# Performance work log

Hardware: AMD Instinct MI355X
Metric: run time of the kernel (lower is better)

## Reference

```python
import jax, jax.numpy as jnp
import numpy as np

H = 0.1           # bandwidth
R = 1024          # pdf_resolution
Q = 2048          # quantile_sample_resolution
EPS = 1e-6
LOG_NORM_SQRT2PI = float(np.log(np.sqrt(2.0 * np.pi)))


def _grid(s):
    # s: (E, Q) samples -> (E, R) linspace(min, max) with 0.0 replaced by 1e-7
    mn = s.min(axis=1)
    mx = s.max(axis=1)
    t = mn[:, None] + (mx - mn)[:, None] * (jnp.arange(R, dtype=s.dtype) / (R - 1))
    return jnp.where(t != 0.0, t, jnp.asarray(1e-7, s.dtype))


def _logpdf(x, locs):
    # x: (E, B) kernel centers; locs: (E, R) eval points
    # log p(t) = logsumexp_b(-0.5 ((t - x_b)/h)^2) - log(B) - log(h * sqrt(2*pi))
    B = x.shape[1]
    z = (locs[:, :, None] - x[:, None, :]) / H          # (E, R, B)
    lse = jax.nn.logsumexp(-0.5 * z * z, axis=-1)       # (E, R)
    return lse - (np.log(B) + np.log(H) + LOG_NORM_SQRT2PI)


def _kde(inputs, bank, noise, comp_idx, sel, slot_idx):
    x = inputs.T                                         # (E, B)
    # mixture sampling: pick component, add Gaussian noise (scale = bandwidth)
    samples = jnp.take_along_axis(x, comp_idx, axis=1) + H * noise   # (E, Q)

    # current pdf over sample range
    t0 = _grid(samples)
    current = jnp.exp(_logpdf(x, t0))                    # (E, R)

    # per-feature bijector branch (0..5; branch 6 'Exp' is unreachable in TF
    # since tf.random.uniform maxval=6 is exclusive)
    selc = sel[:, None]
    s = samples
    s_safe = jnp.where(jnp.abs(s) < EPS, jnp.asarray(EPS, s.dtype), s)
    conds_s = [selc == i for i in range(6)]
    y = jnp.select(conds_s, [
        2.0 * s,                 # Scale(2)
        s - 3.0,                 # Shift(-3)
        1.0 / s_safe,            # Reciprocal
        0.8 * s + 5.0,           # Chain([Shift(5), Scale(0.8)])
        jax.nn.sigmoid(s),       # Sigmoid
        jax.nn.softplus(s),      # Softplus
    ])
    t1 = _grid(y)                                        # (E, R)
    yc01 = jnp.clip(t1, EPS, 1.0 - EPS)                  # safe domain for logit
    ycp = jnp.clip(t1, EPS, None)                        # safe domain for softplus-inv
    conds_t = [selc == i for i in range(6)]
    # inverse f^{-1}(t) per branch
    xi = jnp.select(conds_t, [
        t1 / 2.0,
        t1 + 3.0,
        1.0 / t1,                                        # t1 != 0 by _grid fix
        (t1 - 5.0) / 0.8,
        jnp.log(yc01) - jnp.log1p(-yc01),                # logit
        jnp.log(jnp.expm1(ycp)),                         # softplus inverse
    ])
    # log |d f^{-1} / dt| per branch
    ld = jnp.select(conds_t, [
        jnp.full_like(t1, -np.log(2.0)),
        jnp.zeros_like(t1),
        -2.0 * jnp.log(jnp.abs(t1)),
        jnp.full_like(t1, -np.log(0.8)),
        -jnp.log(yc01) - jnp.log1p(-yc01),
        ycp - jnp.log(jnp.expm1(ycp)),
    ])
    transformed = jnp.exp(_logpdf(x, xi) + ld)           # (E, R)

    # scatter into bank: row 0 <- current, row 1 <- transformed,
    # random slot <- previous row-0 (read before update, as sparse_read(0))
    prev = bank[0]
    out = bank.at[0].set(current).at[1].set(transformed).at[slot_idx].set(prev)
    return out


def setup_inputs() -> dict:
    key = jax.random.key(0)
    k1, k2, k3, k4, k5 = jax.random.split(key, 5)
    inputs = jax.random.normal(k1, (256, 512), dtype=jnp.float32)
    bank = jax.random.normal(k2, (128, 512, 1024), dtype=jnp.float32)
    noise = jax.random.normal(k3, (512, 2048), dtype=jnp.float32)
    comp_idx = jax.random.randint(k4, (512, 2048), 0, 256, dtype=jnp.int32)
    sel = jax.random.randint(k5, (512,), 0, 6, dtype=jnp.int32)
    return {"inputs": inputs, "bank": bank, "noise": noise,
            "comp_idx": comp_idx, "sel": sel, "slot_idx": 37}


def reference(inputs, bank, noise, comp_idx, sel, slot_idx):
    return _kde(inputs, bank, noise, comp_idx, sel, slot_idx)
```

## Files before the change

kernel.cpp:

```cpp
#include <hip/hip_runtime.h>
#include <hip/hip_bf16.h>

#define NQ 2048
#define NB 512
#define NX 256
#define NR 1024
#define KDE_EPS 1e-6f
#define SLOT_ELEMS (NB * NR)
#define LOGC 4.1615308846901885f
#define NORM 0.015583685919813959f

__global__ __launch_bounds__(256) void row_stats(
    const float* __restrict__ inputs,
    const float* __restrict__ noise,
    const int*   __restrict__ comp_idx,
    const int*   __restrict__ sel,
    float* __restrict__ stats)
{
    const int b   = blockIdx.x;
    const int tid = threadIdx.x;
    const int selb = sel[b];

    float mns =  INFINITY, mxs = -INFINITY;
    float mny =  INFINITY, mxy = -INFINITY;

    for (int q = tid; q < NQ; q += 256) {
        const int   idx = comp_idx[b * NQ + q];
        const float nz  = noise[b * NQ + q];
        const float s   = inputs[idx * NB + b] + 0.1f * nz;
        mns = fminf(mns, s);
        mxs = fmaxf(mxs, s);
        const float ssafe = (fabsf(s) < KDE_EPS) ? KDE_EPS : s;
        float y;
        switch (selb) {
            case 0:  y = 2.0f * s; break;
            case 1:  y = s - 3.0f; break;
            case 2:  y = 1.0f / ssafe; break;
            case 3:  y = 0.8f * s + 5.0f; break;
            case 4:  y = 1.0f / (1.0f + __expf(-s)); break;
            default: y = fmaxf(s, 0.0f) + log1pf(__expf(-fabsf(s))); break;
        }
        mny = fminf(mny, y);
        mxy = fmaxf(mxy, y);
    }

    #pragma unroll
    for (int off = 32; off > 0; off >>= 1) {
        mns = fminf(mns, __shfl_down(mns, off, 64));
        mxs = fmaxf(mxs, __shfl_down(mxs, off, 64));
        mny = fminf(mny, __shfl_down(mny, off, 64));
        mxy = fmaxf(mxy, __shfl_down(mxy, off, 64));
    }

    __shared__ float red[4][4];
    const int wave = tid >> 6;
    const int lane = tid & 63;
    if (lane == 0) {
        red[0][wave] = mns; red[1][wave] = mxs;
        red[2][wave] = mny; red[3][wave] = mxy;
    }
    __syncthreads();
    if (tid == 0) {
        float a = red[0][0], c = red[1][0], d = red[2][0], e = red[3][0];
        #pragma unroll
        for (int w = 1; w < 4; ++w) {
            a = fminf(a, red[0][w]);
            c = fmaxf(c, red[1][w]);
            d = fminf(d, red[2][w]);
            e = fmaxf(e, red[3][w]);
        }
        stats[0 * NB + b] = a;
        stats[1 * NB + b] = c;
        stats[2 * NB + b] = d;
        stats[3 * NB + b] = e;
    }
}

__global__ __launch_bounds__(256) void grid_eval(
    const float* __restrict__ inputs,
    const int*   __restrict__ sel,
    const int*   __restrict__ slot_idx_p,
    const float* __restrict__ stats,
    float* __restrict__ out)
{
    const int b     = blockIdx.x;
    const int chunk = blockIdx.y;
    const int tid   = threadIdx.x;

    __shared__ float xs10[NX];
    xs10[tid] = inputs[tid * NB + b] * 10.0f;
    __syncthreads();

    const int   r  = chunk * 256 + tid;
    const float rr = (float)r / 1023.0f;

    const float mns = stats[0 * NB + b];
    const float mxs = stats[1 * NB + b];
    const float mny = stats[2 * NB + b];
    const float mxy = stats[3 * NB + b];

    float t0 = mns + (mxs - mns) * rr;
    if (t0 == 0.0f) t0 = 1e-7f;
    float t1 = mny + (mxy - mny) * rr;
    if (t1 == 0.0f) t1 = 1e-7f;

    const int selb = sel[b];
    const float yc01 = fminf(fmaxf(t1, KDE_EPS), 1.0f - KDE_EPS);
    const float ycp  = fmaxf(t1, KDE_EPS);

    float xi, ld;
    switch (selb) {
        case 0:  xi = 0.5f * t1;            ld = -0.6931471805599453f; break;
        case 1:  xi = t1 + 3.0f;            ld = 0.0f;                 break;
        case 2:  xi = 1.0f / t1;            ld = -2.0f * logf(fabsf(t1)); break;
        case 3:  xi = (t1 - 5.0f) * 1.25f;  ld = 0.22314355131420976f; break;
        case 4:  xi = logf(yc01) - log1pf(-yc01);
                 ld = -logf(yc01) - log1pf(-yc01);                     break;
        default: { const float em = expm1f(ycp);
                   xi = logf(em);
                   ld = ycp - xi; }                                     break;
    }

    const float t010 = t0 * 10.0f;
    const float xi10 = xi * 10.0f;

    float acc0 = 0.0f, acc1 = 0.0f;
    #pragma unroll 8
    for (int j = 0; j < NX; ++j) {
        const float xv = xs10[j];
        const float z0 = t010 - xv;
        const float z1 = xi10 - xv;
        acc0 += __expf(-0.5f * z0 * z0);
        acc1 += __expf(-0.5f * z1 * z1);
    }

    const float current     = acc0 * NORM;
    const float transformed = __expf(__logf(acc1) + ld - LOGC);

    const int slot_idx = *slot_idx_p;
    const size_t o = (size_t)b * NR + r;
    if (slot_idx != 0) out[o] = current;
    if (slot_idx != 1) out[SLOT_ELEMS + o] = transformed;
}

__global__ __launch_bounds__(256) void copy_bank(
    const float4* __restrict__ bank,
    const int*    __restrict__ slot_idx_p,
    float4* __restrict__ out)
{
    const int PER_SLOT_V4 = SLOT_ELEMS / 4;
    const int slot_idx = *slot_idx_p;
    const size_t i = (size_t)blockIdx.x * blockDim.x + threadIdx.x;
    const int slot = (int)(i >> 17);
    const size_t pos = i & (size_t)(PER_SLOT_V4 - 1);
    if (slot == slot_idx) {
        out[i] = bank[pos];
    } else if (slot >= 2) {
        out[i] = bank[i];
    }
}

extern "C" void kernel_launch(void* const* d_in, const int* in_sizes, int n_in,
                              void* d_out, int out_size, void* d_ws, size_t ws_size,
                              hipStream_t stream) {
    const float* inputs   = (const float*)d_in[0];
    const float* bank     = (const float*)d_in[1];
    const float* noise    = (const float*)d_in[2];
    const int*   comp_idx = (const int*)d_in[3];
    const int*   sel      = (const int*)d_in[4];
    const int*   slotp    = (const int*)d_in[5];
    float* out   = (float*)d_out;
    float* stats = (float*)d_ws;

    row_stats<<<NB, 256, 0, stream>>>(inputs, noise, comp_idx, sel, stats);

    dim3 g2(NB, NR / 256);
    grid_eval<<<g2, 256, 0, stream>>>(inputs, sel, slotp, stats, out);

    const int total_v4 = 128 * (SLOT_ELEMS / 4);
    copy_bank<<<total_v4 / 256, 256, 0, stream>>>((const float4*)bank, slotp, (float4*)out);
}
```

Measured before the change: 488.8 us.

## Fuse stats, KDE eval and bank copy into one interleaved kernel

Merges the three kernels into a single launch. Odd blocks do a grid-stride nontemporal bank copy while even blocks compute the row min/max and the KDE grid evaluation, so the memory-bound copy overlaps with the compute-bound evaluation. Each eval block now recomputes the row statistics itself, four times per row, with input lookups taken from shared memory instead of a gather from global memory. This removes two launches and the stats round trip through workspace, at the cost of redundant reduction work.

New measurement: 457.3 us. 1.07x faster.

```diff
diff --git a/kernel.cpp b/kernel.cpp
--- a/kernel.cpp
+++ b/kernel.cpp
@@ -1,5 +1,4 @@
 #include <hip/hip_runtime.h>
-#include <hip/hip_bf16.h>
 
 #define NQ 2048
 #define NB 512
@@ -7,27 +6,74 @@
 #define NR 1024
 #define KDE_EPS 1e-6f
 #define SLOT_ELEMS (NB * NR)
+#define PER_SLOT_V4 (SLOT_ELEMS / 4)
+#define TOTAL_V4 (128 * PER_SLOT_V4)
 #define LOGC 4.1615308846901885f
 #define NORM 0.015583685919813959f
 
-__global__ __launch_bounds__(256) void row_stats(
+#define COPY_BLOCKS 2048
+#define EVAL_BLOCKS 2048
+#define COPY_ITERS (TOTAL_V4 / (COPY_BLOCKS * 256))
+
+typedef float f4 __attribute__((ext_vector_type(4)));
+
+__global__ __launch_bounds__(256) void kde_fused(
     const float* __restrict__ inputs,
+    const f4*    __restrict__ bank,
     const float* __restrict__ noise,
     const int*   __restrict__ comp_idx,
     const int*   __restrict__ sel,
-    float* __restrict__ stats)
+    const int*   __restrict__ slot_idx_p,
+    float* __restrict__ out)
 {
-    const int b   = blockIdx.x;
     const int tid = threadIdx.x;
+    const int bid = blockIdx.x;
+    const int slot_idx = *slot_idx_p;
+
+    if (bid & 1) {
+        const int cb = bid >> 1;
+        f4* o4 = (f4*)out;
+        size_t i = (size_t)cb * 256 + tid;
+        const size_t stride = (size_t)COPY_BLOCKS * 256;
+        #pragma unroll 4
+        for (int it = 0; it < COPY_ITERS; ++it, i += stride) {
+            const int slot = (int)(i >> 17);
+            if (slot == slot_idx) {
+                const size_t pos = i & (size_t)(PER_SLOT_V4 - 1);
+                f4 v = __builtin_nontemporal_load(&bank[pos]);
+                __builtin_nontemporal_store(v, &o4[i]);
+            } else if (slot >= 2) {
+                f4 v = __builtin_nontemporal_load(&bank[i]);
+                __builtin_nontemporal_store(v, &o4[i]);
+            }
+        }
+        return;
+    }
+
+    const int eb    = bid >> 1;
+    const int b     = eb >> 2;
+    const int chunk = eb & 3;
+
+    __shared__ float xsraw[NX];
+    __shared__ float xs10[NX];
+    __shared__ float red[4][4];
+
+    {
+        const float xv = inputs[tid * NB + b];
+        xsraw[tid] = xv;
+        xs10[tid]  = xv * 10.0f;
+    }
+    __syncthreads();
+
     const int selb = sel[b];
 
     float mns =  INFINITY, mxs = -INFINITY;
     float mny =  INFINITY, mxy = -INFINITY;
-
+    #pragma unroll
     for (int q = tid; q < NQ; q += 256) {
         const int   idx = comp_idx[b * NQ + q];
         const float nz  = noise[b * NQ + q];
-        const float s   = inputs[idx * NB + b] + 0.1f * nz;
+        const float s   = xsraw[idx] + 0.1f * nz;
         mns = fminf(mns, s);
         mxs = fmaxf(mxs, s);
         const float ssafe = (fabsf(s) < KDE_EPS) ? KDE_EPS : s;
@@ -51,8 +97,6 @@
         mny = fminf(mny, __shfl_down(mny, off, 64));
         mxy = fmaxf(mxy, __shfl_down(mxy, off, 64));
     }
-
-    __shared__ float red[4][4];
     const int wave = tid >> 6;
     const int lane = tid & 63;
     if (lane == 0) {
@@ -60,51 +104,19 @@
         red[2][wave] = mny; red[3][wave] = mxy;
     }
     __syncthreads();
-    if (tid == 0) {
-        float a = red[0][0], c = red[1][0], d = red[2][0], e = red[3][0];
-        #pragma unroll
-        for (int w = 1; w < 4; ++w) {
-            a = fminf(a, red[0][w]);
-            c = fmaxf(c, red[1][w]);
-            d = fminf(d, red[2][w]);
-            e = fmaxf(e, red[3][w]);
-        }
-        stats[0 * NB + b] = a;
-        stats[1 * NB + b] = c;
-        stats[2 * NB + b] = d;
-        stats[3 * NB + b] = e;
-    }
-}
-
-__global__ __launch_bounds__(256) void grid_eval(
-    const float* __restrict__ inputs,
-    const int*   __restrict__ sel,
-    const int*   __restrict__ slot_idx_p,
-    const float* __restrict__ stats,
-    float* __restrict__ out)
-{
-    const int b     = blockIdx.x;
-    const int chunk = blockIdx.y;
-    const int tid   = threadIdx.x;
-
-    __shared__ float xs10[NX];
-    xs10[tid] = inputs[tid * NB + b] * 10.0f;
-    __syncthreads();
+    mns = fminf(fminf(red[0][0], red[0][1]), fminf(red[0][2], red[0][3]));
+    mxs = fmaxf(fmaxf(red[1][0], red[1][1]), fmaxf(red[1][2], red[1][3]));
+    mny = fminf(fminf(red[2][0], red[2][1]), fminf(red[2][2], red[2][3]));
+    mxy = fmaxf(fmaxf(red[3][0], red[3][1]), fmaxf(red[3][2], red[3][3]));
 
     const int   r  = chunk * 256 + tid;
     const float rr = (float)r / 1023.0f;
-
-    const float mns = stats[0 * NB + b];
-    const float mxs = stats[1 * NB + b];
-    const float mny = stats[2 * NB + b];
-    const float mxy = stats[3 * NB + b];
 
     float t0 = mns + (mxs - mns) * rr;
     if (t0 == 0.0f) t0 = 1e-7f;
     float t1 = mny + (mxy - mny) * rr;
     if (t1 == 0.0f) t1 = 1e-7f;
 
-    const int selb = sel[b];
     const float yc01 = fminf(fmaxf(t1, KDE_EPS), 1.0f - KDE_EPS);
     const float ycp  = fmaxf(t1, KDE_EPS);
 
@@ -137,46 +149,22 @@
     const float current     = acc0 * NORM;
     const float transformed = __expf(__logf(acc1) + ld - LOGC);
 
-    const int slot_idx = *slot_idx_p;
     const size_t o = (size_t)b * NR + r;
     if (slot_idx != 0) out[o] = current;
     if (slot_idx != 1) out[SLOT_ELEMS + o] = transformed;
-}
-
-__global__ __launch_bounds__(256) void copy_bank(
-    const float4* __restrict__ bank,
-    const int*    __restrict__ slot_idx_p,
-    float4* __restrict__ out)
-{
-    const int PER_SLOT_V4 = SLOT_ELEMS / 4;
-    const int slot_idx = *slot_idx_p;
-    const size_t i = (size_t)blockIdx.x * blockDim.x + threadIdx.x;
-    const int slot = (int)(i >> 17);
-    const size_t pos = i & (size_t)(PER_SLOT_V4 - 1);
-    if (slot == slot_idx) {
-        out[i] = bank[pos];
-    } else if (slot >= 2) {
-        out[i] = bank[i];
-    }
 }
 
 extern "C" void kernel_launch(void* const* d_in, const int* in_sizes, int n_in,
                               void* d_out, int out_size, void* d_ws, size_t ws_size,
                               hipStream_t stream) {
     const float* inputs   = (const float*)d_in[0];
-    const float* bank     = (const float*)d_in[1];
+    const f4*    bank     = (const f4*)d_in[1];
     const float* noise    = (const float*)d_in[2];
     const int*   comp_idx = (const int*)d_in[3];
     const int*   sel      = (const int*)d_in[4];
     const int*   slotp    = (const int*)d_in[5];
-    float* out   = (float*)d_out;
-    float* stats = (float*)d_ws;
+    float* out = (float*)d_out;
 
-    row_stats<<<NB, 256, 0, stream>>>(inputs, noise, comp_idx, sel, stats);
-
-    dim3 g2(NB, NR / 256);
-    grid_eval<<<g2, 256, 0, stream>>>(inputs, sel, slotp, stats, out);
-
-    const int total_v4 = 128 * (SLOT_ELEMS / 4);
-    copy_bank<<<total_v4 / 256, 256, 0, stream>>>((const float4*)bank, slotp, (float4*)out);
+    kde_fused<<<COPY_BLOCKS + EVAL_BLOCKS, 256, 0, stream>>>(
+        inputs, bank, noise, comp_idx, sel, slotp, out);
 }
```
